# Performance work log

Hardware: AMD Instinct MI355X
Metric: run time of the kernel (lower is better)

Reference implementation:

```python
import jax, jax.numpy as jnp
import numpy as np

ORDER = 2
C_IN = 32   # per-hop feature dim d
C_OUT = 64


def setup_inputs() -> dict:
    key = jax.random.key(0)
    k = jax.random.split(key, 6)
    b, num_n, num_m, d, t = 2, 512, 256, C_IN, 128
    feat_context = jax.random.normal(k[0], (b, num_n, d, t), dtype=jnp.float32)
    feat_target = jax.random.normal(k[1], (b, num_m, d, t), dtype=jnp.float32)
    adj = jax.random.uniform(k[2], (b, ORDER, num_m, num_n), dtype=jnp.float32)
    missing_mask_context = jax.random.randint(k[3], (b, t, num_n), 0, 2).astype(jnp.float32)
    c_cat = (ORDER + 1) * d  # 96
    W_mlp = jax.random.normal(k[4], (C_OUT, c_cat), dtype=jnp.float32) / np.sqrt(c_cat)
    b_mlp = jax.random.normal(k[5], (C_OUT,), dtype=jnp.float32) * 0.01
    return {"feat_context": feat_context, "feat_target": feat_target, "adj": adj,
            "missing_mask_context": missing_mask_context, "W_mlp": W_mlp, "b_mlp": b_mlp}


def _aggregate(fc_btnd, ft_btmd, adj_bmn, mask_btn):
    # mask out missing context nodes, per (batch, time)
    a = adj_bmn[:, None, :, :] * (1.0 - mask_btn[:, :, None, :])   # [b,t,m,n]
    norm = a / (jnp.sum(a, axis=-1, keepdims=True) + 1.0)          # [b,t,m,n]
    # residual + adjacency-weighted neighbor sum (batched matmul instead of [b,t,m,n,d] blow-up)
    agg = ft_btmd + jnp.einsum('btmn,btnd->btmd', norm, fc_btnd)   # [b,t,m,d]
    return agg


def reference(feat_context, feat_target, adj, missing_mask_context, W_mlp, b_mlp):
    # feat_context: [b,n,d,t], feat_target: [b,m,d,t], adj: [b,k,m,n], mask: [b,t,n]
    fc = jnp.transpose(feat_context, (0, 3, 1, 2))  # [b,t,n,d]
    ft = jnp.transpose(feat_target, (0, 3, 1, 2))   # [b,t,m,d]
    outs = [feat_target]
    for i in range(ORDER):
        agg = _aggregate(fc, ft, adj[:, i], missing_mask_context)      # [b,t,m,d]
        outs.append(jnp.transpose(agg, (0, 2, 3, 1)))                  # [b,m,d,t]
    out = jnp.concatenate(outs, axis=2)  # [b,m,(order+1)*d,t]
    # 1x1 conv over the feature channel dim + ReLU (dropout is identity at eval)
    y = jnp.einsum('bmct,oc->bmot', out, W_mlp) + b_mlp[None, None, :, None]
    return jax.nn.relu(y)  # [b,m,c_out,t]
```

## Files before the change

### kernel.cpp

```cpp
#include <hip/hip_runtime.h>
#include <cstdint>
#include <cstddef>


using shortx8 = __attribute__((ext_vector_type(8))) short;
using floatx4 = __attribute__((ext_vector_type(4))) float;

__device__ __forceinline__ float b2f(unsigned short u) {
    union { unsigned int i; float f; } v; v.i = ((unsigned int)u) << 16; return v.f;
}
__device__ __forceinline__ unsigned short f2b(float f) {
    union { float f; unsigned int i; } v; v.f = f;
    unsigned int x = v.i;
    return (unsigned short)((x + 0x7FFFu + ((x >> 16) & 1u)) >> 16);
}
__device__ __forceinline__ void gl_lds16(const unsigned short* g, unsigned short* l) {
    __builtin_amdgcn_global_load_lds(
        (const __attribute__((address_space(1))) unsigned int*)g,
        (__attribute__((address_space(3))) unsigned int*)l, 16, 0, 0);
}

__global__ void k_adj(const float* __restrict__ adj, unsigned short* __restrict__ adjb) {
    int i4 = (blockIdx.x * 256 + threadIdx.x) * 4;
    float4 v = *(const float4*)(adj + i4);
    ushort4 o;
    o.x = f2b(v.x); o.y = f2b(v.y); o.z = f2b(v.z); o.w = f2b(v.w);
    *(ushort4*)(adjb + i4) = o;
}

__global__ void k_g(const float* __restrict__ fc, const float* __restrict__ mask,
                    unsigned short* __restrict__ gt) {
    const int jb = blockIdx.x, nb = blockIdx.y, b = blockIdx.z;
    const int tid = threadIdx.x;
    const int n0 = nb * 32;
    const int r = tid >> 3, c4 = (tid & 7) * 4;
    if (jb >= 128) {
        const int t0 = (jb - 128) * 32;
        float4 mv = *(const float4*)(mask + ((size_t)b * 128 + t0 + r) * 512 + n0 + c4);
        ushort4 o;
        o.x = f2b(1.f - mv.x); o.y = f2b(1.f - mv.y);
        o.z = f2b(1.f - mv.z); o.w = f2b(1.f - mv.w);
        *(ushort4*)(gt + ((size_t)b * 4224 + 4096 + t0 + r) * 512 + n0 + c4) = o;
        return;
    }
    const int j0 = jb * 32;
    const int t0 = j0 & 127;
    __shared__ float wls[32][33];
    __shared__ unsigned short tls[32][34];
    {
        float4 mv = *(const float4*)(mask + ((size_t)b * 128 + t0 + r) * 512 + n0 + c4);
        wls[r][c4 + 0] = 1.f - mv.x; wls[r][c4 + 1] = 1.f - mv.y;
        wls[r][c4 + 2] = 1.f - mv.z; wls[r][c4 + 3] = 1.f - mv.w;
    }
    float4 fv = *(const float4*)(fc + ((size_t)b * 512 + n0 + r) * 4096 + j0 + c4);
    __syncthreads();
    tls[c4 + 0][r] = f2b(fv.x * wls[c4 + 0][r]);
    tls[c4 + 1][r] = f2b(fv.y * wls[c4 + 1][r]);
    tls[c4 + 2][r] = f2b(fv.z * wls[c4 + 2][r]);
    tls[c4 + 3][r] = f2b(fv.w * wls[c4 + 3][r]);
    __syncthreads();
    ushort4 o;
    o.x = tls[r][c4 + 0]; o.y = tls[r][c4 + 1];
    o.z = tls[r][c4 + 2]; o.w = tls[r][c4 + 3];
    *(ushort4*)(gt + ((size_t)b * 4224 + j0 + r) * 512 + n0 + c4) = o;
}

__launch_bounds__(256, 1)
__global__ void k_gemm(const unsigned short* __restrict__ adjb,
                       const unsigned short* __restrict__ gt,
                       unsigned short* __restrict__ u) {
    const int jt = blockIdx.x, mt = blockIdx.y, bi = blockIdx.z;
    const int b = bi >> 1;
    const int tid = threadIdx.x;
    const int wave = tid >> 6, lane = tid & 63;
    const int l15 = lane & 15, quad = lane >> 4;
    const int wm = wave >> 1, wj = wave & 1;

    __shared__ __align__(16) unsigned short Al[128 * 32];
    __shared__ __align__(16) unsigned short Bl[128 * 32];

    const int srow = lane >> 2;
    const int skq  = (lane & 3) * 8;
    const unsigned short* Ag = adjb + ((size_t)bi * 256 + mt * 128) * 512;
    const unsigned short* Bg = gt   + ((size_t)b * 4224 + jt * 128) * 512;

    floatx4 acc[4][4];
    #pragma unroll
    for (int i = 0; i < 4; ++i)
        #pragma unroll
        for (int j = 0; j < 4; ++j) acc[i][j] = (floatx4){0.f, 0.f, 0.f, 0.f};

    for (int k0 = 0; k0 < 512; k0 += 32) {
        __syncthreads();
        #pragma unroll
        for (int r = 0; r < 2; ++r) {
            const int ch = wave * 2 + r;
            const int row = ch * 16 + srow;
            gl_lds16(Ag + (size_t)row * 512 + k0 + skq, &Al[ch * 512]);
            gl_lds16(Bg + (size_t)row * 512 + k0 + skq, &Bl[ch * 512]);
        }
        __syncthreads();

        shortx8 af[4], bf[4];
        #pragma unroll
        for (int i = 0; i < 4; ++i)
            af[i] = *(const shortx8*)&Al[(wm * 64 + i * 16 + l15) * 32 + quad * 8];
        #pragma unroll
        for (int j = 0; j < 4; ++j)
            bf[j] = *(const shortx8*)&Bl[(wj * 64 + j * 16 + l15) * 32 + quad * 8];
        #pragma unroll
        for (int i = 0; i < 4; ++i)
            #pragma unroll
            for (int j = 0; j < 4; ++j)
                acc[i][j] = __builtin_amdgcn_mfma_f32_16x16x32_bf16(af[i], bf[j], acc[i][j], 0, 0, 0);
    }

    unsigned short* up = u + ((size_t)(bi * 256 + mt * 128 + wm * 64 + quad * 4)) * 4224
                           + jt * 128 + wj * 64 + l15;
    #pragma unroll
    for (int i = 0; i < 4; ++i)
        #pragma unroll
        for (int j = 0; j < 4; ++j)
            #pragma unroll
            for (int reg = 0; reg < 4; ++reg)
                up[(size_t)(i * 16 + reg) * 4224 + j * 16] = f2b(acc[i][j][reg]);
}

__launch_bounds__(256)
__global__ void k_mlp(const float* __restrict__ ft, const unsigned short* __restrict__ u,
                      const float* __restrict__ W, const float* __restrict__ bias,
                      float* __restrict__ y) {
    const int m = blockIdx.x, b = blockIdx.y;
    const int tid = threadIdx.x;
    __shared__ float Xl[96 * 128];
    __shared__ float Wl[64 * 97];
    __shared__ float bl[64];
    __shared__ float r0l[128], r1l[128];

    const unsigned short* up0 = u + ((size_t)(b * 2 + 0) * 256 + m) * 4224;
    const unsigned short* up1 = u + ((size_t)(b * 2 + 1) * 256 + m) * 4224;

    if (tid < 128)       r0l[tid]       = 1.f / (b2f(up0[4096 + tid]) + 1.f);
    else                 r1l[tid - 128] = 1.f / (b2f(up1[4096 + tid - 128]) + 1.f);
    for (int idx = tid; idx < 6144; idx += 256) {
        int o = idx / 96, c = idx - o * 96;
        Wl[o * 97 + c] = W[idx];
    }
    if (tid < 64) bl[tid] = bias[tid];
    __syncthreads();

    {
        const int c  = tid >> 3;
        const int tv = (tid & 7) * 16;
        const float* fp = ft + ((size_t)b * 256 + m) * 4096 + (size_t)c * 128 + tv;
        const unsigned short* q0 = up0 + (size_t)c * 128 + tv;
        const unsigned short* q1 = up1 + (size_t)c * 128 + tv;
        float fv[16];
        *(float4*)(fv + 0)  = *(const float4*)(fp + 0);
        *(float4*)(fv + 4)  = *(const float4*)(fp + 4);
        *(float4*)(fv + 8)  = *(const float4*)(fp + 8);
        *(float4*)(fv + 12) = *(const float4*)(fp + 12);
        uint4 raw0a = *(const uint4*)(q0);
        uint4 raw0b = *(const uint4*)(q0 + 8);
        uint4 raw1a = *(const uint4*)(q1);
        uint4 raw1b = *(const uint4*)(q1 + 8);
        const unsigned short* pu0a = (const unsigned short*)&raw0a;
        const unsigned short* pu0b = (const unsigned short*)&raw0b;
        const unsigned short* pu1a = (const unsigned short*)&raw1a;
        const unsigned short* pu1b = (const unsigned short*)&raw1b;
        float* X1 = &Xl[(size_t)c * 128 + tv];
        float* X2 = &Xl[(size_t)(32 + c) * 128 + tv];
        float* X3 = &Xl[(size_t)(64 + c) * 128 + tv];
        #pragma unroll
        for (int i = 0; i < 16; ++i) {
            float f = fv[i];
            float u0v = b2f(i < 8 ? pu0a[i] : pu0b[i - 8]);
            float u1v = b2f(i < 8 ? pu1a[i] : pu1b[i - 8]);
            X1[i] = f;
            X2[i] = f + u0v * r0l[tv + i];
            X3[i] = f + u1v * r1l[tv + i];
        }
    }
    __syncthreads();

    const int og = tid >> 4, tg = tid & 15, t0 = tg * 8;
    float acc[4][8];
    #pragma unroll
    for (int i = 0; i < 4; ++i) {
        float bv = bl[og * 4 + i];
        #pragma unroll
        for (int k = 0; k < 8; ++k) acc[i][k] = bv;
    }
    for (int c = 0; c < 96; ++c) {
        float x[8];
        *(float4*)(x + 0) = *(const float4*)&Xl[(size_t)c * 128 + t0];
        *(float4*)(x + 4) = *(const float4*)&Xl[(size_t)c * 128 + t0 + 4];
        float w0 = Wl[(og * 4 + 0) * 97 + c];
        float w1 = Wl[(og * 4 + 1) * 97 + c];
        float w2 = Wl[(og * 4 + 2) * 97 + c];
        float w3 = Wl[(og * 4 + 3) * 97 + c];
        #pragma unroll
        for (int k = 0; k < 8; ++k) {
            acc[0][k] += w0 * x[k];
            acc[1][k] += w1 * x[k];
            acc[2][k] += w2 * x[k];
            acc[3][k] += w3 * x[k];
        }
    }
    float* yp = y + (((size_t)b * 256 + m) * 64 + og * 4) * 128 + t0;
    #pragma unroll
    for (int i = 0; i < 4; ++i) {
        float4 pa, pb;
        pa.x = acc[i][0] > 0.f ? acc[i][0] : 0.f;
        pa.y = acc[i][1] > 0.f ? acc[i][1] : 0.f;
        pa.z = acc[i][2] > 0.f ? acc[i][2] : 0.f;
        pa.w = acc[i][3] > 0.f ? acc[i][3] : 0.f;
        pb.x = acc[i][4] > 0.f ? acc[i][4] : 0.f;
        pb.y = acc[i][5] > 0.f ? acc[i][5] : 0.f;
        pb.z = acc[i][6] > 0.f ? acc[i][6] : 0.f;
        pb.w = acc[i][7] > 0.f ? acc[i][7] : 0.f;
        *(float4*)(yp + (size_t)i * 128 + 0) = pa;
        *(float4*)(yp + (size_t)i * 128 + 4) = pb;
    }
}

extern "C" void kernel_launch(void* const* d_in, const int* in_sizes, int n_in,
                              void* d_out, int out_size, void* d_ws, size_t ws_size,
                              hipStream_t stream) {
    const float* fc   = (const float*)d_in[0];
    const float* ft   = (const float*)d_in[1];
    const float* adj  = (const float*)d_in[2];
    const float* mask = (const float*)d_in[3];
    const float* W    = (const float*)d_in[4];
    const float* bias = (const float*)d_in[5];
    float* y = (float*)d_out;

    unsigned short* gt   = (unsigned short*)d_ws;
    unsigned short* adjb = gt + (size_t)2 * 4224 * 512;
    unsigned short* u    = adjb + (size_t)4 * 256 * 512;

    k_adj <<<512, 256, 0, stream>>>(adj, adjb);
    k_g   <<<dim3(132, 16, 2), 256, 0, stream>>>(fc, mask, gt);
    k_gemm<<<dim3(33, 2, 4), 256, 0, stream>>>(adjb, gt, u);
    k_mlp <<<dim3(256, 2), 256, 0, stream>>>(ft, u, W, bias, y);
}
```

Baseline: 115.2 us.

## Fold residual into weights and run the MLP stage on bf16 MFMA

The 1x1-conv MLP now uses bf16 MFMA instructions instead of scalar FP32 FMAs over an LDS tile. The residual feat_target term is folded algebraically into the weights (W1+W2+W3). The GEMM writes its outputs transposed into a [m,t,d] layout so they can feed MFMA B-operands directly, and a new kernel converts feat_target to bf16 in the same layout. This removes the large shared-memory staging and FP32 inner loop, at the cost of an extra launch, bf16 rounding of feat_target and the weights, and scattered 2-byte stores in the GEMM epilogue.

```diff
diff --git a/kernel.cpp b/kernel.cpp
--- a/kernel.cpp
+++ b/kernel.cpp
@@ -20,7 +20,18 @@
         (__attribute__((address_space(3))) unsigned int*)l, 16, 0, 0);
 }
 
-__global__ void k_adj(const float* __restrict__ adj, unsigned short* __restrict__ adjb) {
+__global__ void k_adj(const float* __restrict__ adj, const float* __restrict__ W,
+                      unsigned short* __restrict__ adjb, unsigned short* __restrict__ Wb) {
+    if (blockIdx.x == 512) {
+        for (int e = threadIdx.x; e < 2048; e += 256) {
+            int o = e >> 5, d = e & 31;
+            float w1 = W[o * 96 + d], w2 = W[o * 96 + 32 + d], w3 = W[o * 96 + 64 + d];
+            Wb[e]        = f2b(w1 + w2 + w3);
+            Wb[2048 + e] = f2b(w2);
+            Wb[4096 + e] = f2b(w3);
+        }
+        return;
+    }
     int i4 = (blockIdx.x * 256 + threadIdx.x) * 4;
     float4 v = *(const float4*)(adj + i4);
     ushort4 o;
@@ -65,10 +76,40 @@
     *(ushort4*)(gt + ((size_t)b * 4224 + j0 + r) * 512 + n0 + c4) = o;
 }
 
+__global__ void k_ft(const float* __restrict__ ft, unsigned short* __restrict__ ftT) {
+    const int m = blockIdx.x, b = blockIdx.y;
+    const int tid = threadIdx.x;
+    __shared__ unsigned short l[32][136];
+    const float* src = ft + ((size_t)(b * 256 + m) * 32) * 128;
+    {
+        const int d = tid >> 3, t0 = (tid & 7) * 16;
+        float4 v0 = *(const float4*)(src + (size_t)d * 128 + t0);
+        float4 v1 = *(const float4*)(src + (size_t)d * 128 + t0 + 4);
+        float4 v2 = *(const float4*)(src + (size_t)d * 128 + t0 + 8);
+        float4 v3 = *(const float4*)(src + (size_t)d * 128 + t0 + 12);
+        unsigned short* p = &l[d][t0];
+        p[0]  = f2b(v0.x); p[1]  = f2b(v0.y); p[2]  = f2b(v0.z); p[3]  = f2b(v0.w);
+        p[4]  = f2b(v1.x); p[5]  = f2b(v1.y); p[6]  = f2b(v1.z); p[7]  = f2b(v1.w);
+        p[8]  = f2b(v2.x); p[9]  = f2b(v2.y); p[10] = f2b(v2.z); p[11] = f2b(v2.w);
+        p[12] = f2b(v3.x); p[13] = f2b(v3.y); p[14] = f2b(v3.z); p[15] = f2b(v3.w);
+    }
+    __syncthreads();
+    {
+        const int t = tid & 127, dh = (tid >> 7) * 16;
+        unsigned short tmp[16];
+        #pragma unroll
+        for (int k = 0; k < 16; ++k) tmp[k] = l[dh + k][t];
+        unsigned short* dst = ftT + ((size_t)(b * 256 + m) * 128 + t) * 32 + dh;
+        *(shortx8*)(dst)     = *(const shortx8*)(tmp);
+        *(shortx8*)(dst + 8) = *(const shortx8*)(tmp + 8);
+    }
+}
+
 __launch_bounds__(256, 1)
 __global__ void k_gemm(const unsigned short* __restrict__ adjb,
                        const unsigned short* __restrict__ gt,
-                       unsigned short* __restrict__ u) {
+                       unsigned short* __restrict__ ut,
+                       unsigned short* __restrict__ sbuf) {
     const int jt = blockIdx.x, mt = blockIdx.y, bi = blockIdx.z;
     const int b = bi >> 1;
     const int tid = threadIdx.x;
@@ -115,112 +156,76 @@
                 acc[i][j] = __builtin_amdgcn_mfma_f32_16x16x32_bf16(af[i], bf[j], acc[i][j], 0, 0, 0);
     }
 
-    unsigned short* up = u + ((size_t)(bi * 256 + mt * 128 + wm * 64 + quad * 4)) * 4224
-                           + jt * 128 + wj * 64 + l15;
+    if (jt < 32) {
+        const int d = jt;
+        #pragma unroll
+        for (int i = 0; i < 4; ++i)
+            #pragma unroll
+            for (int j = 0; j < 4; ++j) {
+                const int t_ = wj * 64 + j * 16 + l15;
+                #pragma unroll
+                for (int reg = 0; reg < 4; ++reg) {
+                    const int m_ = mt * 128 + wm * 64 + i * 16 + quad * 4 + reg;
+                    ut[(((size_t)bi * 256 + m_) * 128 + t_) * 32 + d] = f2b(acc[i][j][reg]);
+                }
+            }
+    } else {
+        #pragma unroll
+        for (int i = 0; i < 4; ++i)
+            #pragma unroll
+            for (int j = 0; j < 4; ++j) {
+                const int t_ = wj * 64 + j * 16 + l15;
+                #pragma unroll
+                for (int reg = 0; reg < 4; ++reg) {
+                    const int m_ = mt * 128 + wm * 64 + i * 16 + quad * 4 + reg;
+                    sbuf[((size_t)bi * 256 + m_) * 128 + t_] = f2b(acc[i][j][reg]);
+                }
+            }
+    }
+}
+
+__launch_bounds__(256)
+__global__ void k_mlp(const unsigned short* __restrict__ ftT, const unsigned short* __restrict__ ut,
+                      const unsigned short* __restrict__ sbuf, const unsigned short* __restrict__ Wb,
+                      const float* __restrict__ bias, float* __restrict__ y) {
+    const int m = blockIdx.x, b = blockIdx.y;
+    const int tid = threadIdx.x;
+    const int wave = tid >> 6, lane = tid & 63;
+    const int l15 = lane & 15, quad = lane >> 4;
+
+    const size_t wrow = (size_t)(wave * 16 + l15) * 32 + quad * 8;
+    shortx8 aw = *(const shortx8*)(Wb + wrow);
+    shortx8 a2 = *(const shortx8*)(Wb + 2048 + wrow);
+    shortx8 a3 = *(const shortx8*)(Wb + 4096 + wrow);
+    float bv[4];
     #pragma unroll
-    for (int i = 0; i < 4; ++i)
-        #pragma unroll
-        for (int j = 0; j < 4; ++j)
-            #pragma unroll
-            for (int reg = 0; reg < 4; ++reg)
-                up[(size_t)(i * 16 + reg) * 4224 + j * 16] = f2b(acc[i][j][reg]);
-}
-
-__launch_bounds__(256)
-__global__ void k_mlp(const float* __restrict__ ft, const unsigned short* __restrict__ u,
-                      const float* __restrict__ W, const float* __restrict__ bias,
-                      float* __restrict__ y) {
-    const int m = blockIdx.x, b = blockIdx.y;
-    const int tid = threadIdx.x;
-    __shared__ float Xl[96 * 128];
-    __shared__ float Wl[64 * 97];
-    __shared__ float bl[64];
-    __shared__ float r0l[128], r1l[128];
-
-    const unsigned short* up0 = u + ((size_t)(b * 2 + 0) * 256 + m) * 4224;
-    const unsigned short* up1 = u + ((size_t)(b * 2 + 1) * 256 + m) * 4224;
-
-    if (tid < 128)       r0l[tid]       = 1.f / (b2f(up0[4096 + tid]) + 1.f);
-    else                 r1l[tid - 128] = 1.f / (b2f(up1[4096 + tid - 128]) + 1.f);
-    for (int idx = tid; idx < 6144; idx += 256) {
-        int o = idx / 96, c = idx - o * 96;
-        Wl[o * 97 + c] = W[idx];
-    }
-    if (tid < 64) bl[tid] = bias[tid];
-    __syncthreads();
-
-    {
-        const int c  = tid >> 3;
-        const int tv = (tid & 7) * 16;
-        const float* fp = ft + ((size_t)b * 256 + m) * 4096 + (size_t)c * 128 + tv;
-        const unsigned short* q0 = up0 + (size_t)c * 128 + tv;
-        const unsigned short* q1 = up1 + (size_t)c * 128 + tv;
-        float fv[16];
-        *(float4*)(fv + 0)  = *(const float4*)(fp + 0);
-        *(float4*)(fv + 4)  = *(const float4*)(fp + 4);
-        *(float4*)(fv + 8)  = *(const float4*)(fp + 8);
-        *(float4*)(fv + 12) = *(const float4*)(fp + 12);
-        uint4 raw0a = *(const uint4*)(q0);
-        uint4 raw0b = *(const uint4*)(q0 + 8);
-        uint4 raw1a = *(const uint4*)(q1);
-        uint4 raw1b = *(const uint4*)(q1 + 8);
-        const unsigned short* pu0a = (const unsigned short*)&raw0a;
-        const unsigned short* pu0b = (const unsigned short*)&raw0b;
-        const unsigned short* pu1a = (const unsigned short*)&raw1a;
-        const unsigned short* pu1b = (const unsigned short*)&raw1b;
-        float* X1 = &Xl[(size_t)c * 128 + tv];
-        float* X2 = &Xl[(size_t)(32 + c) * 128 + tv];
-        float* X3 = &Xl[(size_t)(64 + c) * 128 + tv];
-        #pragma unroll
-        for (int i = 0; i < 16; ++i) {
-            float f = fv[i];
-            float u0v = b2f(i < 8 ? pu0a[i] : pu0b[i - 8]);
-            float u1v = b2f(i < 8 ? pu1a[i] : pu1b[i - 8]);
-            X1[i] = f;
-            X2[i] = f + u0v * r0l[tv + i];
-            X3[i] = f + u1v * r1l[tv + i];
+    for (int r = 0; r < 4; ++r) bv[r] = bias[wave * 16 + quad * 4 + r];
+
+    const unsigned short* fp = ftT + ((size_t)(b * 256 + m) * 128) * 32;
+    const unsigned short* u0 = ut + ((size_t)((2 * b + 0) * 256 + m) * 128) * 32;
+    const unsigned short* u1 = ut + ((size_t)((2 * b + 1) * 256 + m) * 128) * 32;
+    const unsigned short* s0 = sbuf + ((size_t)(2 * b + 0) * 256 + m) * 128;
+    const unsigned short* s1 = sbuf + ((size_t)(2 * b + 1) * 256 + m) * 128;
+    float* yp = y + ((size_t)(b * 256 + m) * 64) * 128;
+
+    #pragma unroll
+    for (int tt = 0; tt < 8; ++tt) {
+        const int t = tt * 16 + l15;
+        shortx8 bf = *(const shortx8*)(fp + (size_t)t * 32 + quad * 8);
+        shortx8 b0 = *(const shortx8*)(u0 + (size_t)t * 32 + quad * 8);
+        shortx8 b1 = *(const shortx8*)(u1 + (size_t)t * 32 + quad * 8);
+        floatx4 z = {0.f, 0.f, 0.f, 0.f};
+        floatx4 cw = __builtin_amdgcn_mfma_f32_16x16x32_bf16(aw, bf, z, 0, 0, 0);
+        floatx4 c2 = __builtin_amdgcn_mfma_f32_16x16x32_bf16(a2, b0, z, 0, 0, 0);
+        floatx4 c3 = __builtin_amdgcn_mfma_f32_16x16x32_bf16(a3, b1, z, 0, 0, 0);
+        float r0 = 1.f / (b2f(s0[t]) + 1.f);
+        float r1 = 1.f / (b2f(s1[t]) + 1.f);
+        #pragma unroll
+        for (int r = 0; r < 4; ++r) {
+            const int o = wave * 16 + quad * 4 + r;
+            float v = cw[r] + r0 * c2[r] + r1 * c3[r] + bv[r];
+            yp[(size_t)o * 128 + t] = v > 0.f ? v : 0.f;
         }
-    }
-    __syncthreads();
-
-    const int og = tid >> 4, tg = tid & 15, t0 = tg * 8;
-    float acc[4][8];
-    #pragma unroll
-    for (int i = 0; i < 4; ++i) {
-        float bv = bl[og * 4 + i];
-        #pragma unroll
-        for (int k = 0; k < 8; ++k) acc[i][k] = bv;
-    }
-    for (int c = 0; c < 96; ++c) {
-        float x[8];
-        *(float4*)(x + 0) = *(const float4*)&Xl[(size_t)c * 128 + t0];
-        *(float4*)(x + 4) = *(const float4*)&Xl[(size_t)c * 128 + t0 + 4];
-        float w0 = Wl[(og * 4 + 0) * 97 + c];
-        float w1 = Wl[(og * 4 + 1) * 97 + c];
-        float w2 = Wl[(og * 4 + 2) * 97 + c];
-        float w3 = Wl[(og * 4 + 3) * 97 + c];
-        #pragma unroll
-        for (int k = 0; k < 8; ++k) {
-            acc[0][k] += w0 * x[k];
-            acc[1][k] += w1 * x[k];
-            acc[2][k] += w2 * x[k];
-            acc[3][k] += w3 * x[k];
-        }
-    }
-    float* yp = y + (((size_t)b * 256 + m) * 64 + og * 4) * 128 + t0;
-    #pragma unroll
-    for (int i = 0; i < 4; ++i) {
-        float4 pa, pb;
-        pa.x = acc[i][0] > 0.f ? acc[i][0] : 0.f;
-        pa.y = acc[i][1] > 0.f ? acc[i][1] : 0.f;
-        pa.z = acc[i][2] > 0.f ? acc[i][2] : 0.f;
-        pa.w = acc[i][3] > 0.f ? acc[i][3] : 0.f;
-        pb.x = acc[i][4] > 0.f ? acc[i][4] : 0.f;
-        pb.y = acc[i][5] > 0.f ? acc[i][5] : 0.f;
-        pb.z = acc[i][6] > 0.f ? acc[i][6] : 0.f;
-        pb.w = acc[i][7] > 0.f ? acc[i][7] : 0.f;
-        *(float4*)(yp + (size_t)i * 128 + 0) = pa;
-        *(float4*)(yp + (size_t)i * 128 + 4) = pb;
     }
 }
 
@@ -236,11 +241,15 @@
     float* y = (float*)d_out;
 
     unsigned short* gt   = (unsigned short*)d_ws;
-    unsigned short* adjb = gt + (size_t)2 * 4224 * 512;
-    unsigned short* u    = adjb + (size_t)4 * 256 * 512;
-
-    k_adj <<<512, 256, 0, stream>>>(adj, adjb);
+    unsigned short* adjb = gt   + (size_t)2 * 4224 * 512;
+    unsigned short* ut   = adjb + (size_t)4 * 256 * 512;
+    unsigned short* sbuf = ut   + (size_t)4 * 256 * 128 * 32;
+    unsigned short* ftT  = sbuf + (size_t)4 * 256 * 128;
+    unsigned short* Wb   = ftT  + (size_t)2 * 256 * 128 * 32;
+
+    k_adj <<<513, 256, 0, stream>>>(adj, W, adjb, Wb);
     k_g   <<<dim3(132, 16, 2), 256, 0, stream>>>(fc, mask, gt);
-    k_gemm<<<dim3(33, 2, 4), 256, 0, stream>>>(adjb, gt, u);
-    k_mlp <<<dim3(256, 2), 256, 0, stream>>>(ft, u, W, bias, y);
-}
+    k_ft  <<<dim3(256, 2), 256, 0, stream>>>(ft, ftT);
+    k_gemm<<<dim3(33, 2, 4), 256, 0, stream>>>(adjb, gt, ut, sbuf);
+    k_mlp <<<dim3(256, 2), 256, 0, stream>>>(ftT, ut, sbuf, Wb, bias, y);
+}
```

After: 151.4 us. 1.31x slower.
